# Optimization experiments

Hardware: AMD Instinct MI355X
Metric: run time of the kernel (lower is better)

## Reference

```python
import jax, jax.numpy as jnp
import numpy as np

V, E, F, C, H, L = 12000, 512, 2048, 128, 1024, 49

def setup_inputs() -> dict:
    key = jax.random.key(0)
    ks = jax.random.split(key, 20)
    s = 0.02
    return {
        "captions": jax.random.randint(ks[0], (64, 32), 0, V),
        "features": jax.random.normal(ks[1], (64, L, F), jnp.float32),
        "category_enc": jax.random.normal(ks[2], (64, C), jnp.float32),
        "emb": jax.random.uniform(ks[3], (V, E), jnp.float32, -0.1, 0.1),
        "W_ih": jax.random.normal(ks[4], (4 * H, E + F + C), jnp.float32) * s,
        "b_ih": jnp.zeros((4 * H,), jnp.float32),
        "W_hh": jax.random.normal(ks[5], (4 * H, H), jnp.float32) * s,
        "b_hh": jnp.zeros((4 * H,), jnp.float32),
        "fc_W": jax.random.uniform(ks[6], (V, H), jnp.float32, -0.1, 0.1),
        "fc_b": jnp.zeros((V,), jnp.float32),
        "Wh0": jax.random.normal(ks[7], (H, F), jnp.float32) * s,
        "bh0": jnp.zeros((H,), jnp.float32),
        "Wc0": jax.random.normal(ks[8], (H, F), jnp.float32) * s,
        "bc0": jnp.zeros((H,), jnp.float32),
        "att_W": jax.random.normal(ks[9], (F, H), jnp.float32) * s,
        "att_U": jax.random.normal(ks[10], (H, H), jnp.float32) * s,
        "att_v": jax.random.normal(ks[11], (H,), jnp.float32) * s,
    }

def reference(captions, features, category_enc, emb, W_ih, b_ih, W_hh, b_hh,
              fc_W, fc_b, Wh0, bh0, Wc0, bc0, att_W, att_U, att_v):
    # init hidden/cell from mean-pooled features
    mean_feat = features.mean(axis=1)                      # [B, F]
    h = mean_feat @ Wh0.T + bh0                            # [B, H]
    c = mean_feat @ Wc0.T + bc0                            # [B, H]
    feat_proj = jnp.einsum('blf,fa->bla', features, att_W)  # [B, L, H] precompute
    embed = emb[captions]                                  # [B, T, E]

    def step(carry, x_t):
        h, c = carry
        # Bahdanau additive attention
        e = jnp.tanh(feat_proj + (h @ att_U)[:, None, :])  # [B, L, H]
        score = e @ att_v                                  # [B, L]
        w = jax.nn.softmax(score, axis=-1)                 # [B, L]
        context = jnp.einsum('bl,blf->bf', w, features)    # [B, F]
        x = jnp.concatenate([x_t, context, category_enc], axis=1)
        gates = x @ W_ih.T + b_ih + h @ W_hh.T + b_hh      # [B, 4H]
        i, f, g, o = jnp.split(gates, 4, axis=1)
        c2 = jax.nn.sigmoid(f) * c + jax.nn.sigmoid(i) * jnp.tanh(g)
        h2 = jax.nn.sigmoid(o) * jnp.tanh(c2)              # dropout is identity in eval
        out = h2 @ fc_W.T + fc_b                           # [B, V]
        return (h2, c2), (out, w)

    (_, _), (outs, ws) = jax.lax.scan(step, (h, c), jnp.swapaxes(embed, 0, 1))
    return jnp.swapaxes(outs, 0, 1), jnp.swapaxes(ws, 0, 1)
```

## Files before the change

### kernel.cpp

```cpp
#include <hip/hip_runtime.h>
#include <hip/hip_bf16.h>

#define BB 64
#define TT 32
#define VV 12000
#define EE 512
#define FF 2048
#define CDIM 128
#define HH 1024
#define LL 49
#define XKLEN 2688
#define XGLEN 640

typedef __attribute__((ext_vector_type(8))) short bf16x8;
typedef __attribute__((ext_vector_type(4))) float f32x4;

__device__ __forceinline__ unsigned short bf16_rn(float x) {
  unsigned u = __float_as_uint(x);
  u += 0x7FFFu + ((u >> 16) & 1u);
  return (unsigned short)(u >> 16);
}
__device__ __forceinline__ float bf16_tof(unsigned short h) {
  return __uint_as_float(((unsigned)h) << 16);
}
__device__ __forceinline__ void split2(float x, short& hi, short& lo) {
  unsigned short h = bf16_rn(x);
  float r = x - bf16_tof(h);
  hi = (short)h;
  lo = (short)bf16_rn(r);
}
__device__ __forceinline__ bf16x8 cvt8(const float* f) {
  bf16x8 o;
#pragma unroll
  for (int e = 0; e < 8; ++e) o[e] = (short)bf16_rn(f[e]);
  return o;
}
__device__ __forceinline__ void gload16(const void* g, void* l) {
  __builtin_amdgcn_global_load_lds(
      (const __attribute__((address_space(1))) void*)g,
      (__attribute__((address_space(3))) void*)l, 16, 0, 0);
}

__global__ __launch_bounds__(256) void hupart_k(
    const short* __restrict__ hHi,
    const short* __restrict__ attUt,
    const short* __restrict__ featpB,
    const float* __restrict__ att_v,
    float* __restrict__ partS)
{
  __shared__ float red[4][64][5];
  __shared__ float hu_s[16][17];
  __shared__ float av_s[16];
  const int tid = threadIdx.x;
  const int w = tid >> 6, lane = tid & 63;
  const int r = lane & 15, kg = lane >> 4;
  const int bid = blockIdx.x;
  const int id = (bid & 7) * 32 + (bid >> 3);
  const int nt = id >> 2, mh = id & 3;
  const int kb = w * 256;

  if (tid < 16) av_s[tid] = att_v[nt * 16 + tid];

  const short* wp = attUt + (size_t)(nt * 16 + r) * HH + kb + kg * 8;
  const short* ap = hHi + (size_t)(mh * 16 + r) * HH + kb + kg * 8;
  f32x4 acc = {};
#pragma unroll
  for (int k0 = 0; k0 < 256; k0 += 32) {
    bf16x8 bf = *(const bf16x8*)(wp + k0);
    bf16x8 af = *(const bf16x8*)(ap + k0);
    acc = __builtin_amdgcn_mfma_f32_16x16x32_bf16(af, bf, acc, 0, 0, 0);
  }
#pragma unroll
  for (int q = 0; q < 4; ++q)
    red[w][lane][q] = acc[q];
  __syncthreads();

  {
    const int bl = tid >> 4, a = tid & 15;
    const int sl = (bl >> 2) * 16 + a;
    const int ii = bl & 3;
    hu_s[bl][a] = red[0][sl][ii] + red[1][sl][ii] + red[2][sl][ii] + red[3][sl][ii];
  }
  __syncthreads();

  for (int task = tid; task < 16 * LL; task += 256) {
    const int bl = task / LL, l = task - bl * LL;
    const int b = mh * 16 + bl;
    const short* fp = featpB + ((size_t)nt * 3136 + (size_t)b * LL + l) * 16;
    bf16x8 v0 = *(const bf16x8*)&fp[0];
    bf16x8 v1 = *(const bf16x8*)&fp[8];
    float s = 0.f;
#pragma unroll
    for (int a = 0; a < 8; ++a)
      s += tanhf(bf16_tof((unsigned short)v0[a]) + hu_s[bl][a]) * av_s[a];
#pragma unroll
    for (int a = 0; a < 8; ++a)
      s += tanhf(bf16_tof((unsigned short)v1[a]) + hu_s[bl][8 + a]) * av_s[8 + a];
    partS[(size_t)nt * 3136 + (size_t)mh * 784 + task] = s;
  }
}

__global__ __launch_bounds__(256) void glstm3_k(
    const short* __restrict__ hHi, const short* __restrict__ hLi,
    const short* __restrict__ Whb,
    const short* __restrict__ featCtx,
    const float* __restrict__ partS,
    const float* __restrict__ gxg,
    float* __restrict__ cbuf,
    short* __restrict__ hHo, short* __restrict__ hLo,
    float* __restrict__ w_out, int t)
{
  __shared__ float sw[16][52];
  __shared__ float ctx_p[2][16][72];
  __shared__ float red[3][64][17];
  const int tid = threadIdx.x;
  const int w = tid >> 6, lane = tid & 63;
  const int r = lane & 15, kg = lane >> 4;
  const int bid = blockIdx.x;
  const int id = (bid & 7) * 32 + (bid >> 3);
  const int nt = id >> 2, mq = id & 3;

  for (int idx = tid; idx < 16 * LL; idx += 256) {
    const float* ps = partS + (size_t)mq * 784 + idx;
    float s = 0.f;
#pragma unroll 8
    for (int a = 0; a < 64; ++a) s += ps[(size_t)a * 3136];
    sw[idx / LL][idx % LL] = s;
  }
  __syncthreads();
#pragma unroll
  for (int i = 0; i < 4; ++i) {
    const int bl = w * 4 + i;
    float v = (lane < LL) ? sw[bl][lane] : -1e30f;
    float m = v;
#pragma unroll
    for (int off = 32; off > 0; off >>= 1) m = fmaxf(m, __shfl_xor(m, off));
    float e = (lane < LL) ? expf(v - m) : 0.f;
    float s = e;
#pragma unroll
    for (int off = 32; off > 0; off >>= 1) s += __shfl_xor(s, off);
    float ww = e / s;
    if (lane < LL) {
      sw[bl][lane] = ww;
      if (nt == 0)
        w_out[((size_t)(mq * 16 + bl) * TT + t) * LL + lane] = ww;
    }
  }
  __syncthreads();

  {
    const int bl = tid >> 4, tsub = tid & 15;
    const int e8 = (tsub & 7) * 8, lpar = tsub >> 3;
    const size_t base =
        ((size_t)nt * 3136 + (size_t)(mq * 16 + bl) * LL) * 64 + e8;
    float s[8] = {};
    for (int l = lpar; l < LL; l += 2) {
      bf16x8 v = *(const bf16x8*)&featCtx[base + (size_t)l * 64];
      const float wl = sw[bl][l];
#pragma unroll
      for (int e = 0; e < 8; ++e)
        s[e] += wl * bf16_tof((unsigned short)v[e]);
    }
#pragma unroll
    for (int e = 0; e < 8; ++e)
      ctx_p[lpar][bl][e8 + e] = s[e];
  }

  const int brow = mq * 16 + r;
  f32x4 acc0 = {}, acc1 = {}, acc2 = {}, acc3 = {};
#pragma unroll
  for (int c = 0; c < 8; ++c) {
    const int hk = (w * 8 + c) * 32;
    const short* a_h = hHi + (size_t)brow * HH + hk + kg * 8;
    const short* a_l = hLi + (size_t)brow * HH + hk + kg * 8;
    const short* w0p = Whb + (size_t)(0 * 1024 + nt * 16 + r) * HH + hk + kg * 8;
    const short* w1p = Whb + (size_t)(1 * 1024 + nt * 16 + r) * HH + hk + kg * 8;
    const short* w2p = Whb + (size_t)(2 * 1024 + nt * 16 + r) * HH + hk + kg * 8;
    const short* w3p = Whb + (size_t)(3 * 1024 + nt * 16 + r) * HH + hk + kg * 8;
    bf16x8 af  = *(const bf16x8*)a_h;
    bf16x8 alf = *(const bf16x8*)a_l;
    bf16x8 b0 = *(const bf16x8*)w0p;
    acc0 = __builtin_amdgcn_mfma_f32_16x16x32_bf16(af,  b0, acc0, 0, 0, 0);
    acc0 = __builtin_amdgcn_mfma_f32_16x16x32_bf16(alf, b0, acc0, 0, 0, 0);
    bf16x8 b1 = *(const bf16x8*)w1p;
    acc1 = __builtin_amdgcn_mfma_f32_16x16x32_bf16(af,  b1, acc1, 0, 0, 0);
    acc1 = __builtin_amdgcn_mfma_f32_16x16x32_bf16(alf, b1, acc1, 0, 0, 0);
    bf16x8 b2 = *(const bf16x8*)w2p;
    acc2 = __builtin_amdgcn_mfma_f32_16x16x32_bf16(af,  b2, acc2, 0, 0, 0);
    acc2 = __builtin_amdgcn_mfma_f32_16x16x32_bf16(alf, b2, acc2, 0, 0, 0);
    bf16x8 b3 = *(const bf16x8*)w3p;
    acc3 = __builtin_amdgcn_mfma_f32_16x16x32_bf16(af,  b3, acc3, 0, 0, 0);
    acc3 = __builtin_amdgcn_mfma_f32_16x16x32_bf16(alf, b3, acc3, 0, 0, 0);
  }

  if (w != 0) {
#pragma unroll
    for (int q = 0; q < 4; ++q) {
      red[w - 1][lane][0 * 4 + q] = acc0[q];
      red[w - 1][lane][1 * 4 + q] = acc1[q];
      red[w - 1][lane][2 * 4 + q] = acc2[q];
      red[w - 1][lane][3 * 4 + q] = acc3[q];
    }
  }
  __syncthreads();
  if (w == 0) {
    const int j = nt * 16 + r;
#pragma unroll
    for (int q = 0; q < 4; ++q) {
      const int bl = kg * 4 + q;
      const int b = mq * 16 + bl;
      const float* gx = gxg + ((size_t)t * 64 + b) * 4096;
      float gi = acc0[q] + gx[0 * 1024 + j]
               + ctx_p[0][bl][0 * 16 + r] + ctx_p[1][bl][0 * 16 + r];
      float gf = acc1[q] + gx[1 * 1024 + j]
               + ctx_p[0][bl][1 * 16 + r] + ctx_p[1][bl][1 * 16 + r];
      float gg = acc2[q] + gx[2 * 1024 + j]
               + ctx_p[0][bl][2 * 16 + r] + ctx_p[1][bl][2 * 16 + r];
      float go = acc3[q] + gx[3 * 1024 + j]
               + ctx_p[0][bl][3 * 16 + r] + ctx_p[1][bl][3 * 16 + r];
#pragma unroll
      for (int p = 0; p < 3; ++p) {
        gi += red[p][lane][0 * 4 + q];
        gf += red[p][lane][1 * 4 + q];
        gg += red[p][lane][2 * 4 + q];
        go += red[p][lane][3 * 4 + q];
      }
      float si = 1.f / (1.f + expf(-gi));
      float sf = 1.f / (1.f + expf(-gf));
      float so = 1.f / (1.f + expf(-go));
      const size_t ci = (size_t)b * HH + j;
      float cc = sf * cbuf[ci] + si * tanhf(gg);
      float hh = so * tanhf(cc);
      cbuf[ci] = cc;
      short hi, lo; split2(hh, hi, lo);
      hHo[ci] = hi;
      hLo[ci] = lo;
    }
  }
}

__global__ __launch_bounds__(256) void tgemm2_k(
    const short* __restrict__ A,
    const short* __restrict__ attWt,
    const short* __restrict__ Wctxb,
    short* __restrict__ featpB, short* __restrict__ featCtx)
{
  __shared__ short lA[128 * 32];
  __shared__ short lW[128 * 32];
  const int tid = threadIdx.x;
  const int w = tid >> 6, lane = tid & 63;
  const int r = lane & 15, kg = lane >> 4;
  const int M = BB * LL, K = FF;
  const bool ctx = (blockIdx.y >= 8);
  const short* Wb = ctx ? Wctxb : attWt;
  const int n0 = (ctx ? (blockIdx.y - 8) : blockIdx.y) * 128;
  const int m0 = blockIdx.x * 128;
  const int srow = tid >> 2, scol = (tid & 3) * 8;

  f32x4 acc[2][8] = {};
  for (int k0 = 0; k0 < K; k0 += 32) {
    __syncthreads();
#pragma unroll
    for (int j = 0; j < 2; ++j) {
      const int row = j * 64 + srow;
      int ar = m0 + row; if (ar >= M) ar = M - 1;
      const size_t lbase = (size_t)j * 4096 + (size_t)w * 1024;
      gload16(&A[(size_t)ar * K + k0 + scol], (char*)lA + lbase);
      gload16(&Wb[(size_t)(n0 + row) * K + k0 + scol], (char*)lW + lbase);
    }
    __syncthreads();
    bf16x8 a0 = *(const bf16x8*)&lA[(w * 32 +  0 + r) * 32 + kg * 8];
    bf16x8 a1 = *(const bf16x8*)&lA[(w * 32 + 16 + r) * 32 + kg * 8];
#pragma unroll
    for (int nf = 0; nf < 8; ++nf) {
      bf16x8 wf = *(const bf16x8*)&lW[(nf * 16 + r) * 32 + kg * 8];
      acc[0][nf] = __builtin_amdgcn_mfma_f32_16x16x32_bf16(a0, wf, acc[0][nf], 0, 0, 0);
      acc[1][nf] = __builtin_amdgcn_mfma_f32_16x16x32_bf16(a1, wf, acc[1][nf], 0, 0, 0);
    }
  }
#pragma unroll
  for (int nf = 0; nf < 8; ++nf) {
    const int col = n0 + nf * 16 + r;
#pragma unroll
    for (int mf = 0; mf < 2; ++mf)
#pragma unroll
      for (int q = 0; q < 4; ++q) {
        const int grow = m0 + w * 32 + mf * 16 + kg * 4 + q;
        if (grow < M) {
          const short v = (short)bf16_rn(acc[mf][nf][q]);
          if (!ctx) {
            const int ntc = col >> 4, aa = col & 15;
            featpB[((size_t)ntc * 3136 + grow) * 16 + aa] = v;
          } else {
            const int gate = col >> 10, ntc = (col >> 4) & 63, jj = col & 15;
            featCtx[((size_t)ntc * 3136 + grow) * 64 + gate * 16 + jj] = v;
          }
        }
      }
  }
}

__global__ __launch_bounds__(256) void tgemm3_k(
    const short* __restrict__ Ah, const short* __restrict__ Al,
    const short* __restrict__ Wb, const float* __restrict__ bias,
    float* __restrict__ outs)
{
  __shared__ short lAh[128 * 32];
  __shared__ short lAl[128 * 32];
  __shared__ short lW [128 * 32];
  const int tid = threadIdx.x;
  const int w = tid >> 6, lane = tid & 63;
  const int r = lane & 15, kg = lane >> 4;
  const int m0 = blockIdx.x * 128;
  const int n0 = blockIdx.y * 128;
  const int srow = tid >> 2, scol = (tid & 3) * 8;

  f32x4 acc[2][8] = {};
  for (int k0 = 0; k0 < XGLEN; k0 += 32) {
    __syncthreads();
#pragma unroll
    for (int j = 0; j < 2; ++j) {
      const int row = j * 64 + srow;
      const size_t lbase = (size_t)j * 4096 + (size_t)w * 1024;
      gload16(&Ah[(size_t)(m0 + row) * XGLEN + k0 + scol], (char*)lAh + lbase);
      gload16(&Al[(size_t)(m0 + row) * XGLEN + k0 + scol], (char*)lAl + lbase);
      gload16(&Wb[(size_t)(n0 + row) * XGLEN + k0 + scol], (char*)lW + lbase);
    }
    __syncthreads();
    bf16x8 ah0 = *(const bf16x8*)&lAh[(w * 32 +  0 + r) * 32 + kg * 8];
    bf16x8 ah1 = *(const bf16x8*)&lAh[(w * 32 + 16 + r) * 32 + kg * 8];
    bf16x8 al0 = *(const bf16x8*)&lAl[(w * 32 +  0 + r) * 32 + kg * 8];
    bf16x8 al1 = *(const bf16x8*)&lAl[(w * 32 + 16 + r) * 32 + kg * 8];
#pragma unroll
    for (int nf = 0; nf < 8; ++nf) {
      bf16x8 wf = *(const bf16x8*)&lW[(nf * 16 + r) * 32 + kg * 8];
      acc[0][nf] = __builtin_amdgcn_mfma_f32_16x16x32_bf16(ah0, wf, acc[0][nf], 0, 0, 0);
      acc[0][nf] = __builtin_amdgcn_mfma_f32_16x16x32_bf16(al0, wf, acc[0][nf], 0, 0, 0);
      acc[1][nf] = __builtin_amdgcn_mfma_f32_16x16x32_bf16(ah1, wf, acc[1][nf], 0, 0, 0);
      acc[1][nf] = __builtin_amdgcn_mfma_f32_16x16x32_bf16(al1, wf, acc[1][nf], 0, 0, 0);
    }
  }
#pragma unroll
  for (int nf = 0; nf < 8; ++nf) {
    const int colv = n0 + nf * 16 + r;
    const float bv = bias[colv];
#pragma unroll
    for (int mf = 0; mf < 2; ++mf)
#pragma unroll
      for (int q = 0; q < 4; ++q) {
        const int grow = m0 + w * 32 + mf * 16 + kg * 4 + q;
        outs[(size_t)grow * 4096 + colv] = acc[mf][nf][q] + bv;
      }
  }
}

__global__ __launch_bounds__(256) void bgemm_k(
    const short* __restrict__ Ah, const short* __restrict__ Al,
    const short* __restrict__ Wb, const float* __restrict__ bias,
    float* __restrict__ outs)
{
  __shared__ short lAh[128 * 32];
  __shared__ short lAl[128 * 32];
  __shared__ short lW [128 * 32];
  const int tid = threadIdx.x;
  const int w = tid >> 6, lane = tid & 63;
  const int r = lane & 15, kg = lane >> 4;
  const int m0 = blockIdx.x * 128;
  const int n0 = blockIdx.y * 128;
  const int srow = tid >> 2, scol = (tid & 3) * 8;

  f32x4 acc[2][8] = {};
  for (int k0 = 0; k0 < HH; k0 += 32) {
    __syncthreads();
#pragma unroll
    for (int j = 0; j < 2; ++j) {
      const int row = j * 64 + srow;
      int wr = n0 + row; if (wr >= VV) wr = VV - 1;
      const size_t lbase = (size_t)j * 4096 + (size_t)w * 1024;
      gload16(&Ah[(size_t)(m0 + row) * HH + k0 + scol], (char*)lAh + lbase);
      gload16(&Al[(size_t)(m0 + row) * HH + k0 + scol], (char*)lAl + lbase);
      gload16(&Wb[(size_t)wr * HH + k0 + scol], (char*)lW + lbase);
    }
    __syncthreads();
    bf16x8 ah0 = *(const bf16x8*)&lAh[(w * 32 +  0 + r) * 32 + kg * 8];
    bf16x8 ah1 = *(const bf16x8*)&lAh[(w * 32 + 16 + r) * 32 + kg * 8];
    bf16x8 al0 = *(const bf16x8*)&lAl[(w * 32 +  0 + r) * 32 + kg * 8];
    bf16x8 al1 = *(const bf16x8*)&lAl[(w * 32 + 16 + r) * 32 + kg * 8];
#pragma unroll
    for (int nf = 0; nf < 8; ++nf) {
      bf16x8 wf = *(const bf16x8*)&lW[(nf * 16 + r) * 32 + kg * 8];
      acc[0][nf] = __builtin_amdgcn_mfma_f32_16x16x32_bf16(ah0, wf, acc[0][nf], 0, 0, 0);
      acc[0][nf] = __builtin_amdgcn_mfma_f32_16x16x32_bf16(al0, wf, acc[0][nf], 0, 0, 0);
      acc[1][nf] = __builtin_amdgcn_mfma_f32_16x16x32_bf16(ah1, wf, acc[1][nf], 0, 0, 0);
      acc[1][nf] = __builtin_amdgcn_mfma_f32_16x16x32_bf16(al1, wf, acc[1][nf], 0, 0, 0);
    }
  }
#pragma unroll
  for (int nf = 0; nf < 8; ++nf) {
    const int colv = n0 + nf * 16 + r;
    if (colv < VV) {
      const float bv = bias[colv];
#pragma unroll
      for (int mf = 0; mf < 2; ++mf)
#pragma unroll
        for (int q = 0; q < 4; ++q) {
          const int grow = m0 + w * 32 + mf * 16 + kg * 4 + q;
          const int tt = grow >> 6, b = grow & 63;
          outs[((size_t)b * TT + tt) * VV + colv] = acc[mf][nf][q] + bv;
        }
    }
  }
}

__global__ __launch_bounds__(256) void h0c0_k(
    const short* __restrict__ mfb,
    const short* __restrict__ Wh0b, const float* __restrict__ bh0,
    const short* __restrict__ Wc0b, const float* __restrict__ bc0,
    short* __restrict__ h0H, short* __restrict__ h0L,
    float* __restrict__ cbuf)
{
  const int tid = threadIdx.x;
  const int w = tid >> 6, l = tid & 63;
  const int r = l & 15, kg = l >> 4;
  const bool cpath = blockIdx.x >= 32;
  const int nb = blockIdx.x & 31;
  const short* Wb = cpath ? Wc0b : Wh0b;
  const float* bias = cpath ? bc0 : bh0;
  const int nslice = w >> 1, mbase = (w & 1) * 2;
  const int n0 = nb * 32 + nslice * 16;
  const int nrow = n0 + r;
  const short* wp = Wb + (size_t)nrow * FF + kg * 8;
  const short* ap = mfb + (size_t)(mbase * 16 + r) * FF + kg * 8;
  f32x4 acc[2] = {};
  for (int k0 = 0; k0 < FF; k0 += 32) {
    bf16x8 bf = *(const bf16x8*)(wp + k0);
#pragma unroll
    for (int m = 0; m < 2; ++m) {
      bf16x8 af = *(const bf16x8*)(ap + (size_t)(16 * m) * FF + k0);
      acc[m] = __builtin_amdgcn_mfma_f32_16x16x32_bf16(af, bf, acc[m], 0, 0, 0);
    }
  }
  const float bv = bias[nrow];
#pragma unroll
  for (int m = 0; m < 2; ++m)
#pragma unroll
    for (int q = 0; q < 4; ++q) {
      const int mm = (mbase + m) * 16 + kg * 4 + q;
      const float v = acc[m][q] + bv;
      if (cpath) {
        cbuf[(size_t)mm * HH + nrow] = v;
      } else {
        short hi, lo; split2(v, hi, lo);
        h0H[(size_t)mm * HH + nrow] = hi;
        h0L[(size_t)mm * HH + nrow] = lo;
      }
    }
}

__global__ __launch_bounds__(256) void transpose2_k(
    const float* __restrict__ attU, short* __restrict__ attUt,
    const float* __restrict__ attW, short* __restrict__ attWt)
{
  __shared__ float tile[32][33];
  const bool isW = blockIdx.y >= 32;
  const float* in = isW ? attW : attU;
  short* out = isW ? attWt : attUt;
  const int R = isW ? FF : HH;
  const int br = (isW ? (blockIdx.y - 32) : blockIdx.y) * 32;
  const int bc = blockIdx.x * 32;
  int tx = threadIdx.x & 31, ty4 = (threadIdx.x >> 5) << 2;
#pragma unroll
  for (int i = 0; i < 4; ++i)
    tile[ty4 + i][tx] = in[(size_t)(br + ty4 + i) * HH + bc + tx];
  __syncthreads();
#pragma unroll
  for (int i = 0; i < 4; ++i)
    out[(size_t)(bc + ty4 + i) * R + br + tx] = (short)bf16_rn(tile[tx][ty4 + i]);
}

#define S_FEATB   6422528ULL
#define C1  (S_FEATB)
#define C2  (C1 + 12288000ULL)
#define C3  (C2 + 4194304ULL)
#define C4  (C3 + 2097152ULL)
#define C5  (C4 + 2097152ULL)
#define C6  (C5 + 2621440ULL)
#define C7  (C6 + 8388608ULL)
#define C8  (C7 + 1310720ULL)
#define C9  (C8 + 4096ULL)
#define C10 (C9 + 131072ULL)

__global__ __launch_bounds__(256) void prep_k(
    const float* __restrict__ features, const float* __restrict__ fc_W,
    const float* __restrict__ W_hh, const float* __restrict__ Wh0,
    const float* __restrict__ Wc0, const float* __restrict__ W_ih,
    const int* __restrict__ captions, const float* __restrict__ emb,
    const float* __restrict__ cat,
    const float* __restrict__ b_ih, const float* __restrict__ b_hh,
    short* __restrict__ featb, short* __restrict__ fcWb,
    short* __restrict__ Whb, short* __restrict__ Wh0b,
    short* __restrict__ Wc0b, short* __restrict__ Wxg,
    short* __restrict__ Wctxb, short* __restrict__ xgH,
    short* __restrict__ xgL, float* __restrict__ bg,
    short* __restrict__ mfb)
{
  const size_t stride = (size_t)gridDim.x * 256;
  for (size_t ii = (size_t)blockIdx.x * 256 + threadIdx.x; ii < (C10 >> 3);
       ii += stride) {
    const size_t i = ii << 3;
    float f[8];
    if (i < C1) {
      *(float4*)&f[0] = *(const float4*)&features[i];
      *(float4*)&f[4] = *(const float4*)&features[i + 4];
      *(bf16x8*)&featb[i] = cvt8(f);
    } else if (i < C2) {
      const size_t j = i - C1;
      *(float4*)&f[0] = *(const float4*)&fc_W[j];
      *(float4*)&f[4] = *(const float4*)&fc_W[j + 4];
      *(bf16x8*)&fcWb[j] = cvt8(f);
    } else if (i < C3) {
      const size_t j = i - C2;
      *(float4*)&f[0] = *(const float4*)&W_hh[j];
      *(float4*)&f[4] = *(const float4*)&W_hh[j + 4];
      *(bf16x8*)&Whb[j] = cvt8(f);
    } else if (i < C4) {
      const size_t j = i - C3;
      *(float4*)&f[0] = *(const float4*)&Wh0[j];
      *(float4*)&f[4] = *(const float4*)&Wh0[j + 4];
      *(bf16x8*)&Wh0b[j] = cvt8(f);
    } else if (i < C5) {
      const size_t j = i - C4;
      *(float4*)&f[0] = *(const float4*)&Wc0[j];
      *(float4*)&f[4] = *(const float4*)&Wc0[j + 4];
      *(bf16x8*)&Wc0b[j] = cvt8(f);
    } else if (i < C6) {
      const size_t j = i - C5;
      const int n = (int)(j / XGLEN), k = (int)(j % XGLEN);
      const int ks = (k < EE) ? k : (EE + FF + (k - EE));
      const float* src = &W_ih[(size_t)n * XKLEN + ks];
      *(float4*)&f[0] = *(const float4*)&src[0];
      *(float4*)&f[4] = *(const float4*)&src[4];
      *(bf16x8*)&Wxg[j] = cvt8(f);
    } else if (i < C7) {
      const size_t j = i - C6;
      const int n = (int)(j / FF), k = (int)(j % FF);
      const float* src = &W_ih[(size_t)n * XKLEN + EE + k];
      *(float4*)&f[0] = *(const float4*)&src[0];
      *(float4*)&f[4] = *(const float4*)&src[4];
      *(bf16x8*)&Wctxb[j] = cvt8(f);
    } else if (i < C8) {
      const size_t j = i - C7;
      const int row = (int)(j / XGLEN), k = (int)(j % XGLEN);
      const int t = row >> 6, b = row & 63;
      const float* src;
      if (k < EE) {
        const int cap = captions[b * TT + t];
        src = &emb[(size_t)cap * EE + k];
      } else {
        src = &cat[(size_t)b * CDIM + (k - EE)];
      }
      *(float4*)&f[0] = *(const float4*)&src[0];
      *(float4*)&f[4] = *(const float4*)&src[4];
      bf16x8 hi8, lo8;
#pragma unroll
      for (int e = 0; e < 8; ++e) {
        short h, l2; split2(f[e], h, l2);
        hi8[e] = h; lo8[e] = l2;
      }
      *(bf16x8*)&xgH[j] = hi8;
      *(bf16x8*)&xgL[j] = lo8;
    } else if (i < C9) {
      const size_t j = i - C8;
      float4 a0 = *(const float4*)&b_ih[j];
      float4 a1 = *(const float4*)&b_ih[j + 4];
      float4 c0 = *(const float4*)&b_hh[j];
      float4 c1 = *(const float4*)&b_hh[j + 4];
      float4 o0 = make_float4(a0.x + c0.x, a0.y + c0.y, a0.z + c0.z, a0.w + c0.w);
      float4 o1 = make_float4(a1.x + c1.x, a1.y + c1.y, a1.z + c1.z, a1.w + c1.w);
      *(float4*)&bg[j] = o0;
      *(float4*)&bg[j + 4] = o1;
    } else {
      const size_t j = i - C9;
      const int b = (int)(j >> 11), f0 = (int)(j & 2047);
      float s[8] = {};
      for (int l = 0; l < LL; ++l) {
        const float* src = &features[((size_t)b * LL + l) * FF + f0];
        float4 u0 = *(const float4*)&src[0];
        float4 u1 = *(const float4*)&src[4];
        s[0] += u0.x; s[1] += u0.y; s[2] += u0.z; s[3] += u0.w;
        s[4] += u1.x; s[5] += u1.y; s[6] += u1.z; s[7] += u1.w;
      }
#pragma unroll
      for (int e = 0; e < 8; ++e) s[e] *= (1.f / 49.f);
      *(bf16x8*)&mfb[j] = cvt8(s);
    }
  }
}

extern "C" void kernel_launch(void* const* d_in, const int* in_sizes, int n_in,
                              void* d_out, int out_size, void* d_ws, size_t ws_size,
                              hipStream_t stream) {
  const int*   captions = (const int*)  d_in[0];
  const float* features = (const float*)d_in[1];
  const float* category = (const float*)d_in[2];
  const float* emb      = (const float*)d_in[3];
  const float* W_ih     = (const float*)d_in[4];
  const float* b_ih     = (const float*)d_in[5];
  const float* W_hh     = (const float*)d_in[6];
  const float* b_hh     = (const float*)d_in[7];
  const float* fc_W     = (const float*)d_in[8];
  const float* fc_b     = (const float*)d_in[9];
  const float* Wh0      = (const float*)d_in[10];
  const float* bh0      = (const float*)d_in[11];
  const float* Wc0      = (const float*)d_in[12];
  const float* bc0      = (const float*)d_in[13];
  const float* att_W    = (const float*)d_in[14];
  const float* att_U    = (const float*)d_in[15];
  const float* att_v    = (const float*)d_in[16];

  float* outs  = (float*)d_out;
  float* w_out = outs + (size_t)BB * TT * VV;

  char* p = (char*)d_ws;
  auto alloc = [&](size_t bytes) {
    char* q = p; p += (bytes + 255) & ~(size_t)255; return q;
  };
  short* attUt  = (short*)alloc((size_t)HH * HH * 2);
  short* attWt  = (short*)alloc((size_t)HH * FF * 2);
  short* featb  = (short*)alloc((size_t)BB * LL * FF * 2);
  short* fcWb   = (short*)alloc((size_t)VV * HH * 2);
  short* Wctxb  = (short*)alloc((size_t)4096 * FF * 2);
  short* Whb    = (short*)alloc((size_t)4096 * HH * 2);
  short* Wxg    = (short*)alloc((size_t)4096 * XGLEN * 2);
  short* Wh0b   = (short*)alloc((size_t)HH * FF * 2);
  short* Wc0b   = (short*)alloc((size_t)HH * FF * 2);
  short* mfb    = (short*)alloc((size_t)BB * FF * 2);
  short* h0H    = (short*)alloc((size_t)BB * HH * 2);
  short* h0L    = (short*)alloc((size_t)BB * HH * 2);
  short* xgH    = (short*)alloc((size_t)2048 * XGLEN * 2);
  short* xgL    = (short*)alloc((size_t)2048 * XGLEN * 2);
  short* featpB = (short*)alloc((size_t)64 * 3136 * 16 * 2);
  short* featCtx= (short*)alloc((size_t)64 * 3136 * 64 * 2);
  float* gxg    = (float*)alloc((size_t)2048 * 4096 * 4);
  float* cbuf   = (float*)alloc((size_t)BB * HH * 4);
  float* partS  = (float*)alloc((size_t)64 * 3136 * 4);
  float* bg     = (float*)alloc(4096 * 4);
  short* hallH = featb;
  short* hallL = featb + (size_t)TT * BB * HH;

  prep_k<<<2048, 256, 0, stream>>>(
      features, fc_W, W_hh, Wh0, Wc0, W_ih, captions, emb, category,
      b_ih, b_hh,
      featb, fcWb, Whb, Wh0b, Wc0b, Wxg, Wctxb, xgH, xgL, bg, mfb);
  transpose2_k<<<dim3(32, 96), 256, 0, stream>>>(att_U, attUt, att_W, attWt);
  h0c0_k<<<64, 256, 0, stream>>>(mfb, Wh0b, bh0, Wc0b, bc0, h0H, h0L, cbuf);
  tgemm2_k<<<dim3(25, 40), 256, 0, stream>>>(featb, attWt, Wctxb, featpB, featCtx);
  tgemm3_k<<<dim3(16, 32), 256, 0, stream>>>(xgH, xgL, Wxg, bg, gxg);

  for (int t = 0; t < TT; ++t) {
    const short* hHi = (t == 0) ? h0H : hallH + (size_t)(t - 1) * BB * HH;
    const short* hLi = (t == 0) ? h0L : hallL + (size_t)(t - 1) * BB * HH;
    hupart_k<<<256, 256, 0, stream>>>(
        hHi, attUt, featpB, att_v, partS);
    glstm3_k<<<256, 256, 0, stream>>>(
        hHi, hLi, Whb, featCtx, partS, gxg, cbuf,
        hallH + (size_t)t * BB * HH, hallL + (size_t)t * BB * HH, w_out, t);
  }

  bgemm_k<<<dim3(16, 94), 256, 0, stream>>>(hallH, hallL, fcWb, fc_b, outs);
}
```

Before: 1.744 ms.

## Move W_hh recurrent GEMM into attention-score kernel to run concurrently

The h@W_hh gate GEMM is moved out of the LSTM-cell kernel into the first per-step kernel, which now launches 512 blocks: half compute attention partial scores and half compute the recurrent gate preactivations into a new global buffer. The second kernel then only reduces scores, does softmax and context, and applies the cell update using the stored gate values. This lets the two independent matmuls occupy the GPU at once instead of serialising the W_hh GEMM behind the softmax and context work. In exchange it adds a global round trip for the gate preactivations and makes the first kernel larger.

```diff
diff --git a/kernel.cpp b/kernel.cpp
--- a/kernel.cpp
+++ b/kernel.cpp
@@ -41,70 +41,136 @@
       (__attribute__((address_space(3))) void*)l, 16, 0, 0);
 }
 
-__global__ __launch_bounds__(256) void hupart_k(
-    const short* __restrict__ hHi,
+__global__ __launch_bounds__(256) void step1_k(
+    const short* __restrict__ hHi, const short* __restrict__ hLi,
     const short* __restrict__ attUt,
     const short* __restrict__ featpB,
     const float* __restrict__ att_v,
-    float* __restrict__ partS)
-{
-  __shared__ float red[4][64][5];
+    const short* __restrict__ Whb,
+    float* __restrict__ partS,
+    float* __restrict__ ghh)
+{
+  __shared__ float red4[4][64][5];
   __shared__ float hu_s[16][17];
   __shared__ float av_s[16];
+  __shared__ float red3[3][64][17];
   const int tid = threadIdx.x;
   const int w = tid >> 6, lane = tid & 63;
   const int r = lane & 15, kg = lane >> 4;
-  const int bid = blockIdx.x;
-  const int id = (bid & 7) * 32 + (bid >> 3);
-  const int nt = id >> 2, mh = id & 3;
-  const int kb = w * 256;
-
-  if (tid < 16) av_s[tid] = att_v[nt * 16 + tid];
-
-  const short* wp = attUt + (size_t)(nt * 16 + r) * HH + kb + kg * 8;
-  const short* ap = hHi + (size_t)(mh * 16 + r) * HH + kb + kg * 8;
-  f32x4 acc = {};
-#pragma unroll
-  for (int k0 = 0; k0 < 256; k0 += 32) {
-    bf16x8 bf = *(const bf16x8*)(wp + k0);
-    bf16x8 af = *(const bf16x8*)(ap + k0);
-    acc = __builtin_amdgcn_mfma_f32_16x16x32_bf16(af, bf, acc, 0, 0, 0);
-  }
-#pragma unroll
-  for (int q = 0; q < 4; ++q)
-    red[w][lane][q] = acc[q];
-  __syncthreads();
-
-  {
-    const int bl = tid >> 4, a = tid & 15;
-    const int sl = (bl >> 2) * 16 + a;
-    const int ii = bl & 3;
-    hu_s[bl][a] = red[0][sl][ii] + red[1][sl][ii] + red[2][sl][ii] + red[3][sl][ii];
-  }
-  __syncthreads();
-
-  for (int task = tid; task < 16 * LL; task += 256) {
-    const int bl = task / LL, l = task - bl * LL;
-    const int b = mh * 16 + bl;
-    const short* fp = featpB + ((size_t)nt * 3136 + (size_t)b * LL + l) * 16;
-    bf16x8 v0 = *(const bf16x8*)&fp[0];
-    bf16x8 v1 = *(const bf16x8*)&fp[8];
-    float s = 0.f;
-#pragma unroll
-    for (int a = 0; a < 8; ++a)
-      s += tanhf(bf16_tof((unsigned short)v0[a]) + hu_s[bl][a]) * av_s[a];
-#pragma unroll
-    for (int a = 0; a < 8; ++a)
-      s += tanhf(bf16_tof((unsigned short)v1[a]) + hu_s[bl][8 + a]) * av_s[8 + a];
-    partS[(size_t)nt * 3136 + (size_t)mh * 784 + task] = s;
-  }
-}
-
-__global__ __launch_bounds__(256) void glstm3_k(
-    const short* __restrict__ hHi, const short* __restrict__ hLi,
-    const short* __restrict__ Whb,
+
+  if (blockIdx.x < 256) {
+    const int bid = blockIdx.x;
+    const int id = (bid & 7) * 32 + (bid >> 3);
+    const int nt = id >> 2, mh = id & 3;
+    const int kb = w * 256;
+
+    if (tid < 16) av_s[tid] = att_v[nt * 16 + tid];
+
+    const short* wp = attUt + (size_t)(nt * 16 + r) * HH + kb + kg * 8;
+    const short* ap = hHi + (size_t)(mh * 16 + r) * HH + kb + kg * 8;
+    f32x4 acc = {};
+#pragma unroll
+    for (int k0 = 0; k0 < 256; k0 += 32) {
+      bf16x8 bf = *(const bf16x8*)(wp + k0);
+      bf16x8 af = *(const bf16x8*)(ap + k0);
+      acc = __builtin_amdgcn_mfma_f32_16x16x32_bf16(af, bf, acc, 0, 0, 0);
+    }
+#pragma unroll
+    for (int q = 0; q < 4; ++q)
+      red4[w][lane][q] = acc[q];
+    __syncthreads();
+
+    {
+      const int bl = tid >> 4, a = tid & 15;
+      const int sl = (bl >> 2) * 16 + a;
+      const int ii = bl & 3;
+      hu_s[bl][a] = red4[0][sl][ii] + red4[1][sl][ii]
+                  + red4[2][sl][ii] + red4[3][sl][ii];
+    }
+    __syncthreads();
+
+    for (int task = tid; task < 16 * LL; task += 256) {
+      const int bl = task / LL, l = task - bl * LL;
+      const int b = mh * 16 + bl;
+      const short* fp = featpB + ((size_t)nt * 3136 + (size_t)b * LL + l) * 16;
+      bf16x8 v0 = *(const bf16x8*)&fp[0];
+      bf16x8 v1 = *(const bf16x8*)&fp[8];
+      float s = 0.f;
+#pragma unroll
+      for (int a = 0; a < 8; ++a)
+        s += tanhf(bf16_tof((unsigned short)v0[a]) + hu_s[bl][a]) * av_s[a];
+#pragma unroll
+      for (int a = 0; a < 8; ++a)
+        s += tanhf(bf16_tof((unsigned short)v1[a]) + hu_s[bl][8 + a]) * av_s[8 + a];
+      partS[(size_t)nt * 3136 + (size_t)mh * 784 + task] = s;
+    }
+  } else {
+    const int bid = blockIdx.x - 256;
+    const int id = (bid & 7) * 32 + (bid >> 3);
+    const int nt = id >> 2, mq = id & 3;
+    const int brow = mq * 16 + r;
+    f32x4 acc0 = {}, acc1 = {}, acc2 = {}, acc3 = {};
+#pragma unroll
+    for (int c = 0; c < 8; ++c) {
+      const int hk = (w * 8 + c) * 32;
+      const short* a_h = hHi + (size_t)brow * HH + hk + kg * 8;
+      const short* a_l = hLi + (size_t)brow * HH + hk + kg * 8;
+      const short* w0p = Whb + (size_t)(0 * 1024 + nt * 16 + r) * HH + hk + kg * 8;
+      const short* w1p = Whb + (size_t)(1 * 1024 + nt * 16 + r) * HH + hk + kg * 8;
+      const short* w2p = Whb + (size_t)(2 * 1024 + nt * 16 + r) * HH + hk + kg * 8;
+      const short* w3p = Whb + (size_t)(3 * 1024 + nt * 16 + r) * HH + hk + kg * 8;
+      bf16x8 af  = *(const bf16x8*)a_h;
+      bf16x8 alf = *(const bf16x8*)a_l;
+      bf16x8 b0 = *(const bf16x8*)w0p;
+      acc0 = __builtin_amdgcn_mfma_f32_16x16x32_bf16(af,  b0, acc0, 0, 0, 0);
+      acc0 = __builtin_amdgcn_mfma_f32_16x16x32_bf16(alf, b0, acc0, 0, 0, 0);
+      bf16x8 b1 = *(const bf16x8*)w1p;
+      acc1 = __builtin_amdgcn_mfma_f32_16x16x32_bf16(af,  b1, acc1, 0, 0, 0);
+      acc1 = __builtin_amdgcn_mfma_f32_16x16x32_bf16(alf, b1, acc1, 0, 0, 0);
+      bf16x8 b2 = *(const bf16x8*)w2p;
+      acc2 = __builtin_amdgcn_mfma_f32_16x16x32_bf16(af,  b2, acc2, 0, 0, 0);
+      acc2 = __builtin_amdgcn_mfma_f32_16x16x32_bf16(alf, b2, acc2, 0, 0, 0);
+      bf16x8 b3 = *(const bf16x8*)w3p;
+      acc3 = __builtin_amdgcn_mfma_f32_16x16x32_bf16(af,  b3, acc3, 0, 0, 0);
+      acc3 = __builtin_amdgcn_mfma_f32_16x16x32_bf16(alf, b3, acc3, 0, 0, 0);
+    }
+    if (w != 0) {
+#pragma unroll
+      for (int q = 0; q < 4; ++q) {
+        red3[w - 1][lane][0 * 4 + q] = acc0[q];
+        red3[w - 1][lane][1 * 4 + q] = acc1[q];
+        red3[w - 1][lane][2 * 4 + q] = acc2[q];
+        red3[w - 1][lane][3 * 4 + q] = acc3[q];
+      }
+    }
+    __syncthreads();
+    if (w == 0) {
+      const int j = nt * 16 + r;
+#pragma unroll
+      for (int q = 0; q < 4; ++q) {
+        const int b = mq * 16 + kg * 4 + q;
+        float g0 = acc0[q], g1 = acc1[q], g2 = acc2[q], g3 = acc3[q];
+#pragma unroll
+        for (int p = 0; p < 3; ++p) {
+          g0 += red3[p][lane][0 * 4 + q];
+          g1 += red3[p][lane][1 * 4 + q];
+          g2 += red3[p][lane][2 * 4 + q];
+          g3 += red3[p][lane][3 * 4 + q];
+        }
+        float* gh = ghh + (size_t)b * 4096;
+        gh[0 * 1024 + j] = g0;
+        gh[1 * 1024 + j] = g1;
+        gh[2 * 1024 + j] = g2;
+        gh[3 * 1024 + j] = g3;
+      }
+    }
+  }
+}
+
+__global__ __launch_bounds__(256) void step2_k(
     const short* __restrict__ featCtx,
     const float* __restrict__ partS,
+    const float* __restrict__ ghh,
     const float* __restrict__ gxg,
     float* __restrict__ cbuf,
     short* __restrict__ hHo, short* __restrict__ hLo,
@@ -112,10 +178,8 @@
 {
   __shared__ float sw[16][52];
   __shared__ float ctx_p[2][16][72];
-  __shared__ float red[3][64][17];
   const int tid = threadIdx.x;
   const int w = tid >> 6, lane = tid & 63;
-  const int r = lane & 15, kg = lane >> 4;
   const int bid = blockIdx.x;
   const int id = (bid & 7) * 32 + (bid >> 3);
   const int nt = id >> 2, mq = id & 3;
@@ -165,77 +229,32 @@
     for (int e = 0; e < 8; ++e)
       ctx_p[lpar][bl][e8 + e] = s[e];
   }
-
-  const int brow = mq * 16 + r;
-  f32x4 acc0 = {}, acc1 = {}, acc2 = {}, acc3 = {};
-#pragma unroll
-  for (int c = 0; c < 8; ++c) {
-    const int hk = (w * 8 + c) * 32;
-    const short* a_h = hHi + (size_t)brow * HH + hk + kg * 8;
-    const short* a_l = hLi + (size_t)brow * HH + hk + kg * 8;
-    const short* w0p = Whb + (size_t)(0 * 1024 + nt * 16 + r) * HH + hk + kg * 8;
-    const short* w1p = Whb + (size_t)(1 * 1024 + nt * 16 + r) * HH + hk + kg * 8;
-    const short* w2p = Whb + (size_t)(2 * 1024 + nt * 16 + r) * HH + hk + kg * 8;
-    const short* w3p = Whb + (size_t)(3 * 1024 + nt * 16 + r) * HH + hk + kg * 8;
-    bf16x8 af  = *(const bf16x8*)a_h;
-    bf16x8 alf = *(const bf16x8*)a_l;
-    bf16x8 b0 = *(const bf16x8*)w0p;
-    acc0 = __builtin_amdgcn_mfma_f32_16x16x32_bf16(af,  b0, acc0, 0, 0, 0);
-    acc0 = __builtin_amdgcn_mfma_f32_16x16x32_bf16(alf, b0, acc0, 0, 0, 0);
-    bf16x8 b1 = *(const bf16x8*)w1p;
-    acc1 = __builtin_amdgcn_mfma_f32_16x16x32_bf16(af,  b1, acc1, 0, 0, 0);
-    acc1 = __builtin_amdgcn_mfma_f32_16x16x32_bf16(alf, b1, acc1, 0, 0, 0);
-    bf16x8 b2 = *(const bf16x8*)w2p;
-    acc2 = __builtin_amdgcn_mfma_f32_16x16x32_bf16(af,  b2, acc2, 0, 0, 0);
-    acc2 = __builtin_amdgcn_mfma_f32_16x16x32_bf16(alf, b2, acc2, 0, 0, 0);
-    bf16x8 b3 = *(const bf16x8*)w3p;
-    acc3 = __builtin_amdgcn_mfma_f32_16x16x32_bf16(af,  b3, acc3, 0, 0, 0);
-    acc3 = __builtin_amdgcn_mfma_f32_16x16x32_bf16(alf, b3, acc3, 0, 0, 0);
-  }
-
-  if (w != 0) {
-#pragma unroll
-    for (int q = 0; q < 4; ++q) {
-      red[w - 1][lane][0 * 4 + q] = acc0[q];
-      red[w - 1][lane][1 * 4 + q] = acc1[q];
-      red[w - 1][lane][2 * 4 + q] = acc2[q];
-      red[w - 1][lane][3 * 4 + q] = acc3[q];
-    }
-  }
   __syncthreads();
-  if (w == 0) {
-    const int j = nt * 16 + r;
-#pragma unroll
-    for (int q = 0; q < 4; ++q) {
-      const int bl = kg * 4 + q;
-      const int b = mq * 16 + bl;
-      const float* gx = gxg + ((size_t)t * 64 + b) * 4096;
-      float gi = acc0[q] + gx[0 * 1024 + j]
-               + ctx_p[0][bl][0 * 16 + r] + ctx_p[1][bl][0 * 16 + r];
-      float gf = acc1[q] + gx[1 * 1024 + j]
-               + ctx_p[0][bl][1 * 16 + r] + ctx_p[1][bl][1 * 16 + r];
-      float gg = acc2[q] + gx[2 * 1024 + j]
-               + ctx_p[0][bl][2 * 16 + r] + ctx_p[1][bl][2 * 16 + r];
-      float go = acc3[q] + gx[3 * 1024 + j]
-               + ctx_p[0][bl][3 * 16 + r] + ctx_p[1][bl][3 * 16 + r];
-#pragma unroll
-      for (int p = 0; p < 3; ++p) {
-        gi += red[p][lane][0 * 4 + q];
-        gf += red[p][lane][1 * 4 + q];
-        gg += red[p][lane][2 * 4 + q];
-        go += red[p][lane][3 * 4 + q];
-      }
-      float si = 1.f / (1.f + expf(-gi));
-      float sf = 1.f / (1.f + expf(-gf));
-      float so = 1.f / (1.f + expf(-go));
-      const size_t ci = (size_t)b * HH + j;
-      float cc = sf * cbuf[ci] + si * tanhf(gg);
-      float hh = so * tanhf(cc);
-      cbuf[ci] = cc;
-      short hi, lo; split2(hh, hi, lo);
-      hHo[ci] = hi;
-      hLo[ci] = lo;
-    }
+
+  {
+    const int bl = tid >> 4, jr = tid & 15;
+    const int b = mq * 16 + bl;
+    const int j = nt * 16 + jr;
+    const float* gh = ghh + (size_t)b * 4096;
+    const float* gx = gxg + ((size_t)t * 64 + b) * 4096;
+    float gi = gh[0 * 1024 + j] + gx[0 * 1024 + j]
+             + ctx_p[0][bl][0 * 16 + jr] + ctx_p[1][bl][0 * 16 + jr];
+    float gf = gh[1 * 1024 + j] + gx[1 * 1024 + j]
+             + ctx_p[0][bl][1 * 16 + jr] + ctx_p[1][bl][1 * 16 + jr];
+    float gg = gh[2 * 1024 + j] + gx[2 * 1024 + j]
+             + ctx_p[0][bl][2 * 16 + jr] + ctx_p[1][bl][2 * 16 + jr];
+    float go = gh[3 * 1024 + j] + gx[3 * 1024 + j]
+             + ctx_p[0][bl][3 * 16 + jr] + ctx_p[1][bl][3 * 16 + jr];
+    float si = 1.f / (1.f + expf(-gi));
+    float sf = 1.f / (1.f + expf(-gf));
+    float so = 1.f / (1.f + expf(-go));
+    const size_t ci = (size_t)b * HH + j;
+    float cc = sf * cbuf[ci] + si * tanhf(gg);
+    float hh = so * tanhf(cc);
+    cbuf[ci] = cc;
+    short hi, lo; split2(hh, hi, lo);
+    hHo[ci] = hi;
+    hLo[ci] = lo;
   }
 }
 
@@ -642,6 +661,7 @@
   short* featpB = (short*)alloc((size_t)64 * 3136 * 16 * 2);
   short* featCtx= (short*)alloc((size_t)64 * 3136 * 64 * 2);
   float* gxg    = (float*)alloc((size_t)2048 * 4096 * 4);
+  float* ghh    = (float*)alloc((size_t)64 * 4096 * 4);
   float* cbuf   = (float*)alloc((size_t)BB * HH * 4);
   float* partS  = (float*)alloc((size_t)64 * 3136 * 4);
   float* bg     = (float*)alloc(4096 * 4);
@@ -660,10 +680,10 @@
   for (int t = 0; t < TT; ++t) {
     const short* hHi = (t == 0) ? h0H : hallH + (size_t)(t - 1) * BB * HH;
     const short* hLi = (t == 0) ? h0L : hallL + (size_t)(t - 1) * BB * HH;
-    hupart_k<<<256, 256, 0, stream>>>(
-        hHi, attUt, featpB, att_v, partS);
-    glstm3_k<<<256, 256, 0, stream>>>(
-        hHi, hLi, Whb, featCtx, partS, gxg, cbuf,
+    step1_k<<<512, 256, 0, stream>>>(
+        hHi, hLi, attUt, featpB, att_v, Whb, partS, ghh);
+    step2_k<<<256, 256, 0, stream>>>(
+        featCtx, partS, ghh, gxg, cbuf,
         hallH + (size_t)t * BB * HH, hallL + (size_t)t * BB * HH, w_out, t);
   }
 
```

Result: faster. 1.582 ms (-9.3%).
